# Performance work log

Hardware: AMD Instinct MI355X
Metric: run time of the kernel (lower is better)

The kernel has to match this reference:

```python
import jax, jax.numpy as jnp
import numpy as np

B, S, D = 1, 2048, 1024
F = 1408            # expert intermediate dim
E = 16              # num experts
K = 2               # top_k
CAP_FACTOR = 1.25


def _mlp(h, wg, wu, wd):
    # DeepSeek-style gated MLP (SwiGLU, no bias)
    return (jax.nn.silu(h @ wg) * (h @ wu)) @ wd


def setup_inputs() -> dict:
    key = jax.random.key(0)
    ks = jax.random.split(key, 10)
    sd = 0.02
    return {
        "x": jax.random.normal(ks[0], (B, S, D), jnp.float32),
        "router_w": jax.random.normal(ks[1], (D, E), jnp.float32) * sd,
        "router_b": jnp.zeros((E,), jnp.float32),
        "w_gate": jax.random.normal(ks[2], (E, D, F), jnp.float32) * sd,
        "w_up": jax.random.normal(ks[3], (E, D, F), jnp.float32) * sd,
        "w_down": jax.random.normal(ks[4], (E, F, D), jnp.float32) * sd,
        "sw_gate": jax.random.normal(ks[5], (D, F), jnp.float32) * sd,
        "sw_up": jax.random.normal(ks[6], (D, F), jnp.float32) * sd,
        "sw_down": jax.random.normal(ks[7], (F, D), jnp.float32) * sd,
    }


def reference(x, router_w, router_b, w_gate, w_up, w_down, sw_gate, sw_up, sw_down):
    b, s, d = x.shape
    N = b * s
    NK = N * K
    C = int(np.ceil(CAP_FACTOR * NK / E))  # per-expert capacity

    x_tokens = x.reshape(N, d)

    # Router: softmax -> top-k -> renormalize
    logits = x_tokens @ router_w + router_b           # [N, E]
    probs = jax.nn.softmax(logits, axis=-1)
    vals, idx = jax.lax.top_k(probs, K)               # [N, K]
    vals = vals / (jnp.sum(vals, axis=-1, keepdims=True) + 1e-9)
    idx_flat = idx.reshape(NK)                        # int expert ids
    vals_flat = vals.reshape(NK)

    # Position within each expert's buffer = rank in flattened (token, k) order.
    # Same math as (cumsum(one_hot)*one_hot).sum(-1)-1 in the original.
    oh_e = jax.nn.one_hot(idx_flat, E, dtype=x.dtype)             # [NK, E] (small)
    pos = (jnp.cumsum(oh_e, axis=0) * oh_e).sum(axis=1) - 1       # [NK]
    within = (pos < C).astype(x.dtype)                            # capacity mask
    pos_c = jnp.clip(pos, 0, C - 1).astype(jnp.int32)

    # Dispatch: scatter tokens into per-expert buffers. Positions are unique
    # per expert, so scatter-add equals the dense one-hot einsum exactly.
    token_ids = jnp.arange(NK) // K
    x_pair = x_tokens[token_ids] * within[:, None]                # [NK, D]
    expert_inputs = jnp.zeros((E, C, d), x.dtype).at[idx_flat, pos_c].add(x_pair)

    # Grouped expert MLPs
    expert_outputs = jax.vmap(_mlp)(expert_inputs, w_gate, w_up, w_down)  # [E, C, D]

    # Combine: gather back and weight by renormalized router probs
    gathered = expert_outputs[idx_flat, pos_c] * (vals_flat * within)[:, None]
    output_tokens = gathered.reshape(N, K, d).sum(axis=1)         # [N, D]

    return x + _mlp(x, sw_gate, sw_up, sw_down) + output_tokens.reshape(b, s, d)
```

## Files before the change

kernel.cpp:

```cpp
#include <hip/hip_runtime.h>
#include <hip/hip_bf16.h>

#define TOKENS 2048
#define DIM    1024
#define FDIM   1408
#define NEXP   16
#define NK     (TOKENS * 2)
#define CAP    320
#define RPAD   384

typedef __attribute__((ext_vector_type(4))) float f32x4;
typedef __attribute__((ext_vector_type(2))) float f32x2;
typedef __attribute__((ext_vector_type(8))) short s16x8;
typedef __attribute__((ext_vector_type(4))) short s16x4;

__device__ __forceinline__ short f2bf(float f) {
    unsigned int u = __float_as_uint(f);
    u += 0x7FFFu + ((u >> 16) & 1u);
    return (short)(u >> 16);
}
__device__ __forceinline__ float bf2f(short s) {
    return __uint_as_float(((unsigned int)(unsigned short)s) << 16);
}
__device__ __forceinline__ unsigned int f2bf_pk(float lo, float hi) {
    union { __hip_bfloat162 h; unsigned int u; } c;
    c.h = __float22bfloat162_rn(make_float2(lo, hi));
    return c.u;
}

#define GLDS16(gp, lp) __builtin_amdgcn_global_load_lds(                     \
    (const __attribute__((address_space(1))) unsigned int*)(gp),             \
    (__attribute__((address_space(3))) unsigned int*)(lp), 16, 0, 0)

struct GSegF {
    const short* A; long aStride; int aRpad;
    const float* B0; const float* B1; long bStride;
    short* Out; long oStride; int oRpad;
    const int* cnt; int Mb, Nb, N, K, nblocks;
};
struct GSegB {
    const short* A; long aStride; int aRpad;
    const short* B0; long bStride;
    short* Out; long oStride;
    const int* cnt; int Mb, Nb, N, K, nblocks;
};
struct WSeg { const float* in; short* out; int K, N, mats, nblocks; };

__device__ void wchunk_dev(const WSeg& W, int bid)
{
    const int spm = W.K >> 3;
    const int mat = bid / spm, s = bid % spm;
    const float* in  = W.in  + (size_t)mat * W.K * W.N + (size_t)s * 8 * W.N;
    short* out = W.out + (size_t)mat * W.K * W.N + (size_t)s * W.N * 8;
    const int t = threadIdx.x;
    const int iters = (W.N + 511) >> 9;
    for (int it = 0; it < iters; it++) {
        const int n = it * 512 + 2 * t;
        if (n >= W.N) break;
        const float* src = in + n;
        s16x8 o0, o1;
#pragma unroll
        for (int j = 0; j < 8; j++) {
            float2 v = *(const float2*)(src + (size_t)j * W.N);
            o0[j] = f2bf(v.x);
            o1[j] = f2bf(v.y);
        }
        *(s16x8*)(out + (size_t)n * 8)     = o0;
        *(s16x8*)(out + (size_t)n * 8 + 8) = o1;
    }
}

__device__ void router_dev(const float* __restrict__ x, const float* __restrict__ rw,
                           const float* __restrict__ rb, int* __restrict__ idx_flat,
                           float* __restrict__ vals_flat, int bid)
{
    __shared__ float lg[16][17];
    const int t  = threadIdx.x;
    const int tl = t >> 4;
    const int e  = t & 15;
    const int token = bid * 16 + tl;
    const float* xr = x + (size_t)token * DIM;

    float acc = 0.f;
    for (int d4 = 0; d4 < DIM / 4; d4++) {
        float4 xv = *(const float4*)(xr + d4 * 4);
        acc += xv.x * rw[(d4 * 4 + 0) * NEXP + e];
        acc += xv.y * rw[(d4 * 4 + 1) * NEXP + e];
        acc += xv.z * rw[(d4 * 4 + 2) * NEXP + e];
        acc += xv.w * rw[(d4 * 4 + 3) * NEXP + e];
    }
    lg[tl][e] = acc + rb[e];
    __syncthreads();

    if (t < 16) {
        float l[16];
#pragma unroll
        for (int j = 0; j < 16; j++) l[j] = lg[t][j];
        float m = l[0];
#pragma unroll
        for (int j = 1; j < 16; j++) m = fmaxf(m, l[j]);
        float p[16], den = 0.f;
#pragma unroll
        for (int j = 0; j < 16; j++) { p[j] = __expf(l[j] - m); den += p[j]; }
        int i1 = -1; float b1 = -1e30f;
#pragma unroll
        for (int j = 0; j < 16; j++) if (p[j] > b1) { b1 = p[j]; i1 = j; }
        int i2 = -1; float b2 = -1e30f;
#pragma unroll
        for (int j = 0; j < 16; j++) if (j != i1 && p[j] > b2) { b2 = p[j]; i2 = j; }
        float v1 = b1 / den, v2 = b2 / den;
        float s = v1 + v2 + 1e-9f;
        int tok = bid * 16 + t;
        idx_flat[tok * 2 + 0] = i1;
        idx_flat[tok * 2 + 1] = i2;
        vals_flat[tok * 2 + 0] = v1 / s;
        vals_flat[tok * 2 + 1] = v2 / s;
    }
}

__device__ void xconv_dev(const float* __restrict__ x, short* __restrict__ xb, int bid)
{
    const int token = bid * 2 + (threadIdx.x >> 7);
    const int c = threadIdx.x & 127;
    const float* src = x + (size_t)token * DIM + c * 8;
    float4 v0 = *(const float4*)(src);
    float4 v1 = *(const float4*)(src + 4);
    s16x8 o;
    o[0] = f2bf(v0.x); o[1] = f2bf(v0.y); o[2] = f2bf(v0.z); o[3] = f2bf(v0.w);
    o[4] = f2bf(v1.x); o[5] = f2bf(v1.y); o[6] = f2bf(v1.z); o[7] = f2bf(v1.w);
    *(s16x8*)(xb + (size_t)c * (TOKENS * 8) + (size_t)token * 8) = o;
}

__global__ __launch_bounds__(256) void rx_kernel(
    const float* __restrict__ x, const float* __restrict__ rw,
    const float* __restrict__ rb, int* __restrict__ idx_flat,
    float* __restrict__ vals, short* __restrict__ xb)
{
    int bid = blockIdx.x;
    if (bid < TOKENS / 16) { router_dev(x, rw, rb, idx_flat, vals, bid); return; }
    xconv_dev(x, xb, bid - TOKENS / 16);
}

__global__ void scan_kernel(const int* __restrict__ idx_flat,
                            const float* __restrict__ vals,
                            int* __restrict__ dst, float* __restrict__ wgt,
                            int* __restrict__ cnt)
{
    const int lane = threadIdx.x;
    int base[16];
#pragma unroll
    for (int e = 0; e < 16; e++) base[e] = 0;

    for (int c = 0; c < NK / 64; c++) {
        int i = c * 64 + lane;
        int e = idx_flat[i];
        unsigned long long m[16];
#pragma unroll
        for (int ee = 0; ee < 16; ee++) m[ee] = __ballot(e == ee);
        unsigned long long mym = 0ULL; int myb = 0;
#pragma unroll
        for (int ee = 0; ee < 16; ee++) {
            bool sel = (e == ee);
            mym = sel ? m[ee] : mym;
            myb = sel ? base[ee] : myb;
        }
        int pos = myb + (int)__popcll(mym & ((1ULL << lane) - 1ULL));
        bool within = pos < CAP;
        dst[i] = within ? (e * RPAD + pos) : -1;
        wgt[i] = within ? vals[i] : 0.f;
#pragma unroll
        for (int ee = 0; ee < 16; ee++) base[ee] += (int)__popcll(m[ee]);
    }
    if (lane < 16) cnt[lane] = base[lane] < CAP ? base[lane] : CAP;
}

__global__ __launch_bounds__(256) void scatter_kernel(
    const float* __restrict__ x, const int* __restrict__ dst,
    const int* __restrict__ idx_flat, short* __restrict__ ex)
{
    const int i = blockIdx.x * 2 + (threadIdx.x >> 7);
    const int d0 = dst[i];
    if (d0 < 0) return;
    const int e = idx_flat[i];
    const int pos = d0 - e * RPAD;
    const int token = i >> 1;
    const int c = threadIdx.x & 127;
    const float* src = x + (size_t)token * DIM + c * 8;
    float4 v0 = *(const float4*)(src);
    float4 v1 = *(const float4*)(src + 4);
    s16x8 o;
    o[0] = f2bf(v0.x); o[1] = f2bf(v0.y); o[2] = f2bf(v0.z); o[3] = f2bf(v0.w);
    o[4] = f2bf(v1.x); o[5] = f2bf(v1.y); o[6] = f2bf(v1.z); o[7] = f2bf(v1.w);
    *(s16x8*)(ex + (size_t)e * (DIM * RPAD) + (size_t)c * (RPAD * 8) +
              (size_t)pos * 8) = o;
}

template <int NMAT>
__device__ void gemm_fused_dev(const GSegF& S, int bid)
{
    constexpr int BUFS = 4096 * (1 + NMAT);
    __shared__ short lds[2 * BUFS];

    const int cpx = S.nblocks >> 3;
    const int lid = (bid & 7) * cpx + (bid >> 3);
    const int mb  = lid % S.Mb;
    const int t1  = lid / S.Mb;
    const int nb  = t1 % S.Nb;
    const int g   = t1 / S.Nb;
    const int m0 = mb * 128, n0 = nb * 128;
    if (S.cnt != nullptr && m0 >= S.cnt[g]) return;

    const int tid = threadIdx.x, lane = tid & 63, w = tid >> 6;
    const int wr = w >> 1, wc = w & 1, ln = lane & 15, kg = lane >> 4;
    const int N = S.N, K = S.K;

    const short* Ag  = S.A  + (size_t)g * S.aStride + (size_t)m0 * 8;
    const float* Bg0 = S.B0 + (size_t)g * S.bStride + n0;
    const float* Bg1 = nullptr;
    if constexpr (NMAT == 2) Bg1 = S.B1 + (size_t)g * S.bStride + n0;

    const size_t aR8 = (size_t)S.aRpad * 8;

    const int srow = tid & 127, sslab = tid >> 7;
    const short* aS0 = Ag + sslab * aR8 + srow * 8;
    const short* aS1 = Ag + (2 + sslab) * aR8 + srow * 8;
    const int dA0 = w * 512, dA1 = 2048 + w * 512;

    const float* bSrc;
    int rB, cW;
    if constexpr (NMAT == 2) {
        const int c4 = tid & 31, gq = (tid >> 5) & 3, mat = tid >> 7;
        bSrc = (mat ? Bg1 : Bg0) + (size_t)gq * 8 * N + c4 * 4;
        rB = 4096 + mat * 4096 + gq * 1024;
        cW = c4;
    } else {
        const int c2 = tid & 63, gq = tid >> 6;
        bSrc = Bg0 + (size_t)gq * 8 * N + c2 * 2;
        rB = 4096 + gq * 1024;
        cW = c2;
    }

    f32x4 bq[8];
    f32x2 bd[8];

    auto LOADB = [&](int ks) {
        const float* p = bSrc + (size_t)ks * 32 * N;
        if constexpr (NMAT == 2) {
#pragma unroll
            for (int j = 0; j < 8; j++) bq[j] = *(const f32x4*)(p + (size_t)j * N);
        } else {
#pragma unroll
            for (int j = 0; j < 8; j++) bd[j] = *(const f32x2*)(p + (size_t)j * N);
        }
    };
    auto STGA = [&](int buf, int ks) {
        const size_t ka = (size_t)ks * 4 * aR8;
        short* base = lds + buf * BUFS;
        GLDS16(aS0 + ka, base + dA0);
        GLDS16(aS1 + ka, base + dA1);
    };
    auto WRITEB = [&](int buf) {
        short* d = lds + buf * BUFS + rB;
        if constexpr (NMAT == 2) {
#pragma unroll
            for (int j = 0; j < 4; j++) {
                const int colS = (cW * 4 + j) ^ ((cW >> 1) & 7);
                uint4 o;
                o.x = f2bf_pk(bq[0][j], bq[1][j]);
                o.y = f2bf_pk(bq[2][j], bq[3][j]);
                o.z = f2bf_pk(bq[4][j], bq[5][j]);
                o.w = f2bf_pk(bq[6][j], bq[7][j]);
                *(uint4*)(d + colS * 8) = o;
            }
        } else {
#pragma unroll
            for (int j = 0; j < 2; j++) {
                const int colS = (cW * 2 + j) ^ ((cW >> 2) & 7);
                uint4 o;
                o.x = f2bf_pk(bd[0][j], bd[1][j]);
                o.y = f2bf_pk(bd[2][j], bd[3][j]);
                o.z = f2bf_pk(bd[4][j], bd[5][j]);
                o.w = f2bf_pk(bd[6][j], bd[7][j]);
                *(uint4*)(d + colS * 8) = o;
            }
        }
    };

    const int aO = kg * 1024 + (wr * 64 + ln) * 8;

    f32x4 acc[NMAT][4][4] = {};
    const int nt = K / 32;

    LOADB(0);
    __builtin_amdgcn_sched_barrier(0);
    STGA(0, 0);
    __builtin_amdgcn_sched_barrier(0);
    WRITEB(0);
    __builtin_amdgcn_sched_barrier(0);
    LOADB(1);
    __builtin_amdgcn_sched_barrier(0);
    asm volatile("s_waitcnt lgkmcnt(0)" ::: "memory");
    STGA(1, 1);
    __builtin_amdgcn_sched_barrier(0);

    int cur = 0;
    for (int ks = 0; ks < nt; ks++) {
        if (ks + 1 < nt) asm volatile("s_waitcnt vmcnt(10)" ::: "memory");
        else             asm volatile("s_waitcnt vmcnt(0)"  ::: "memory");
        __builtin_amdgcn_s_barrier();
        __builtin_amdgcn_sched_barrier(0);

        const short* base = lds + cur * BUFS;
        s16x8 af[4];
#pragma unroll
        for (int m = 0; m < 4; m++)
            af[m] = *(const s16x8*)(base + aO + m * 128);
        s16x8 bf[NMAT][4];
#pragma unroll
        for (int nf = 0; nf < 4; nf++) {
            const int col  = wc * 64 + nf * 16 + ln;
            const int colS = col ^ ((col >> 3) & 7);
#pragma unroll
            for (int mat = 0; mat < NMAT; mat++)
                bf[mat][nf] = *(const s16x8*)(base + 4096 + mat * 4096 +
                                              kg * 1024 + colS * 8);
        }

#pragma unroll
        for (int nf = 0; nf < 4; nf++)
#pragma unroll
            for (int m = 0; m < 4; m++)
#pragma unroll
                for (int mat = 0; mat < NMAT; mat++)
                    acc[mat][m][nf] = __builtin_amdgcn_mfma_f32_16x16x32_bf16(
                        af[m], bf[mat][nf], acc[mat][m][nf], 0, 0, 0);

        if (ks + 1 < nt) WRITEB(cur ^ 1);

        __builtin_amdgcn_sched_barrier(0);
        if (ks + 2 < nt) LOADB(ks + 2);
        __builtin_amdgcn_sched_barrier(0);
        asm volatile("s_waitcnt lgkmcnt(0)" ::: "memory");
        __builtin_amdgcn_s_barrier();

        if (ks + 2 < nt) {
            STGA(cur, ks + 2);
            __builtin_amdgcn_sched_barrier(0);
        }
        cur ^= 1;
    }

#pragma unroll
    for (int m = 0; m < 4; m++) {
#pragma unroll
        for (int nf = 0; nf < 4; nf++) {
            const int row = m0 + wr * 64 + m * 16 + kg * 4;
            const int col = n0 + wc * 64 + nf * 16 + ln;
#pragma unroll
            for (int j = 0; j < 4; j++) {
                if constexpr (NMAT == 2) {
                    float gv = acc[0][m][nf][j];
                    float uv = acc[1][m][nf][j];
                    float v = gv / (1.f + __expf(-gv)) * uv;
                    S.Out[(size_t)g * S.oStride + (size_t)(col >> 3) * (S.oRpad * 8) +
                          (size_t)(row + j) * 8 + (col & 7)] = f2bf(v);
                } else {
                    S.Out[(size_t)g * S.oStride + (size_t)(row + j) * N + col] =
                        f2bf(acc[0][m][nf][j]);
                }
            }
        }
    }
}

__device__ void gemm_glds64_dev(const GSegB& S, int bid)
{
    constexpr int BUFS = 6144;
    __shared__ short lds[2 * BUFS];

    const int cpx = S.nblocks >> 3;
    const int lid = (bid & 7) * cpx + (bid >> 3);
    const int mb  = lid % S.Mb;
    const int t1  = lid / S.Mb;
    const int nb  = t1 % S.Nb;
    const int g   = t1 / S.Nb;
    const int m0 = mb * 64, n0 = nb * 128;
    if (S.cnt != nullptr && m0 >= S.cnt[g]) return;

    const int tid = threadIdx.x, lane = tid & 63, w = tid >> 6;
    const int wr = w >> 1, wc = w & 1, ln = lane & 15, kg = lane >> 4;
    const int N = S.N, K = S.K;

    const short* Ag = S.A  + (size_t)g * S.aStride + (size_t)m0 * 8;
    const short* Bg = S.B0 + (size_t)g * S.bStride + (size_t)n0 * 8;

    const size_t aR8 = (size_t)S.aRpad * 8;
    const size_t n8  = (size_t)N * 8;

    const short* aS  = Ag + (size_t)(tid >> 6) * aR8 + (size_t)(tid & 63) * 8;
    const short* bS0 = Bg + (size_t)(tid >> 7) * n8 + (size_t)(tid & 127) * 8;
    const short* bS1 = Bg + (size_t)((tid >> 7) + 2) * n8 + (size_t)(tid & 127) * 8;

    const int dA  = w * 512;
    const int dB0 = 2048 + w * 512;
    const int dB1 = 4096 + w * 512;

    auto STG = [&](int buf, int ks) {
        const size_t ka = (size_t)ks * 4 * aR8;
        const size_t kb = (size_t)ks * 4 * n8;
        short* base = lds + buf * BUFS;
        GLDS16(aS + ka,  base + dA);
        GLDS16(bS0 + kb, base + dB0);
        GLDS16(bS1 + kb, base + dB1);
    };

    const int aO = kg * 512 + (wr * 32 + ln) * 8;
    const int bO = 2048 + kg * 1024 + (wc * 64 + ln) * 8;

    f32x4 acc[2][4] = {};
    const int nt = K / 32;
    STG(0, 0); STG(1, 1);
    int cur = 0;
    for (int ks = 0; ks < nt; ks++) {
        if (ks + 1 < nt) asm volatile("s_waitcnt vmcnt(3)" ::: "memory");
        else             asm volatile("s_waitcnt vmcnt(0)" ::: "memory");
        __builtin_amdgcn_s_barrier();
        __builtin_amdgcn_sched_barrier(0);

        const short* base = lds + cur * BUFS;
        s16x8 af[2];
        af[0] = *(const s16x8*)(base + aO);
        af[1] = *(const s16x8*)(base + aO + 128);
        s16x8 bf[4];
#pragma unroll
        for (int nf = 0; nf < 4; nf++)
            bf[nf] = *(const s16x8*)(base + bO + nf * 128);

#pragma unroll
        for (int nf = 0; nf < 4; nf++)
#pragma unroll
            for (int m = 0; m < 2; m++)
                acc[m][nf] = __builtin_amdgcn_mfma_f32_16x16x32_bf16(
                    af[m], bf[nf], acc[m][nf], 0, 0, 0);

        __builtin_amdgcn_sched_barrier(0);
        __builtin_amdgcn_s_barrier();
        if (ks + 2 < nt) STG(cur, ks + 2);
        cur ^= 1;
    }

#pragma unroll
    for (int m = 0; m < 2; m++) {
#pragma unroll
        for (int nf = 0; nf < 4; nf++) {
            const int row = m0 + wr * 32 + m * 16 + kg * 4;
            const int col = n0 + wc * 64 + nf * 16 + ln;
#pragma unroll
            for (int j = 0; j < 4; j++)
                S.Out[(size_t)g * S.oStride + (size_t)(row + j) * N + col] =
                    f2bf(acc[m][nf][j]);
        }
    }
}

__global__ __launch_bounds__(256, 2) void gateup_kernel(GSegF s0, GSegF s1,
                                                        WSeg w0, WSeg w1)
{
    int bid = blockIdx.x;
    if (bid < s0.nblocks) { gemm_fused_dev<2>(s0, bid); return; }
    bid -= s0.nblocks;
    if (bid < s1.nblocks) { gemm_fused_dev<2>(s1, bid); return; }
    bid -= s1.nblocks;
    if (bid < w0.nblocks) { wchunk_dev(w0, bid); return; }
    wchunk_dev(w1, bid - w0.nblocks);
}

__global__ __launch_bounds__(256, 4) void down_kernel(GSegB s0, GSegB s1)
{
    int bid = blockIdx.x;
    if (bid < s0.nblocks) { gemm_glds64_dev(s0, bid); return; }
    gemm_glds64_dev(s1, bid - s0.nblocks);
}

__global__ __launch_bounds__(256) void combine_kernel(
    const float* __restrict__ x, const short* __restrict__ shout,
    const short* __restrict__ eout, const int* __restrict__ dst,
    const float* __restrict__ wgt, float* __restrict__ out)
{
    const int t = blockIdx.x;
    const int d = threadIdx.x * 4;
    size_t o = (size_t)t * DIM + d;
    float4 xv = *(const float4*)(x + o);
    s16x4 sv = *(const s16x4*)(shout + o);
    float r0 = xv.x + bf2f(sv[0]);
    float r1 = xv.y + bf2f(sv[1]);
    float r2 = xv.z + bf2f(sv[2]);
    float r3 = xv.w + bf2f(sv[3]);
#pragma unroll
    for (int k = 0; k < 2; k++) {
        int di = dst[t * 2 + k];
        if (di >= 0) {
            float wv = wgt[t * 2 + k];
            s16x4 ev = *(const s16x4*)(eout + (size_t)di * DIM + d);
            r0 += wv * bf2f(ev[0]);
            r1 += wv * bf2f(ev[1]);
            r2 += wv * bf2f(ev[2]);
            r3 += wv * bf2f(ev[3]);
        }
    }
    float4 rv = {r0, r1, r2, r3};
    *(float4*)(out + o) = rv;
}

extern "C" void kernel_launch(void* const* d_in, const int* in_sizes, int n_in,
                              void* d_out, int out_size, void* d_ws, size_t ws_size,
                              hipStream_t stream)
{
    const float* x   = (const float*)d_in[0];
    const float* rw  = (const float*)d_in[1];
    const float* rb  = (const float*)d_in[2];
    const float* wg  = (const float*)d_in[3];
    const float* wu  = (const float*)d_in[4];
    const float* wd  = (const float*)d_in[5];
    const float* swg = (const float*)d_in[6];
    const float* swu = (const float*)d_in[7];
    const float* swd = (const float*)d_in[8];
    float* out = (float*)d_out;

    char* wp = (char*)d_ws;
    auto alloc = [&](size_t b) { char* p = wp; wp += (b + 255) & ~(size_t)255; return p; };
    int*   idx_flat = (int*)alloc((size_t)NK * 4);
    float* vals     = (float*)alloc((size_t)NK * 4);
    int*   dst      = (int*)alloc((size_t)NK * 4);
    float* wgt      = (float*)alloc((size_t)NK * 4);
    int*   cnt      = (int*)alloc(64);
    short* xb       = (short*)alloc((size_t)TOKENS * DIM * 2);
    short* ex       = (short*)alloc((size_t)NEXP * RPAD * DIM * 2);
    short* acte     = (short*)alloc((size_t)NEXP * RPAD * FDIM * 2);
    short* acts     = (short*)alloc((size_t)TOKENS * FDIM * 2);
    short* eout     = (short*)alloc((size_t)NEXP * RPAD * DIM * 2);
    short* shout    = (short*)alloc((size_t)TOKENS * DIM * 2);
    short* wdC      = (short*)alloc((size_t)NEXP * DIM * FDIM * 2);
    short* swdC     = (short*)alloc((size_t)DIM * FDIM * 2);

    rx_kernel<<<TOKENS / 16 + TOKENS / 2, 256, 0, stream>>>(x, rw, rb,
                                                            idx_flat, vals, xb);
    scan_kernel<<<1, 64, 0, stream>>>(idx_flat, vals, dst, wgt, cnt);

    scatter_kernel<<<NK / 2, 256, 0, stream>>>(x, dst, idx_flat, ex);

    GSegF segGE = {ex, (long)RPAD * DIM, RPAD, wg, wu, (long)DIM * FDIM,
                   acte, (long)RPAD * FDIM, RPAD, cnt, 3, 11, FDIM, DIM, 3 * 11 * NEXP};
    GSegF segGS = {xb, 0L, TOKENS, swg, swu, 0L,
                   acts, 0L, TOKENS, nullptr, 16, 11, FDIM, DIM, 16 * 11};
    WSeg Wd  = {wd,  wdC,  FDIM, DIM, NEXP, NEXP * (FDIM / 8)};
    WSeg Wsd = {swd, swdC, FDIM, DIM, 1,    FDIM / 8};
    gateup_kernel<<<segGE.nblocks + segGS.nblocks + Wd.nblocks + Wsd.nblocks,
                    256, 0, stream>>>(segGE, segGS, Wd, Wsd);

    GSegB segDE = {acte, (long)RPAD * FDIM, RPAD, wdC, (long)DIM * FDIM,
                   eout, (long)RPAD * DIM, cnt, 6, 8, DIM, FDIM, 6 * 8 * NEXP};
    GSegB segDS = {acts, 0L, TOKENS, swdC, 0L,
                   shout, 0L, nullptr, 32, 8, DIM, FDIM, 32 * 8};
    down_kernel<<<segDE.nblocks + segDS.nblocks, 256, 0, stream>>>(segDE, segDS);

    combine_kernel<<<TOKENS, 256, 0, stream>>>(x, shout, eout, dst, wgt, out);
}
```

Measured before the change: 230.7 us.

## Split fused gate/up GEMM into separate GEMMs plus standalone SiLU kernel

Replaces the dual-matrix fused gate/up GEMM, which computed SiLU(gate)*up in its epilogue, with single-matrix GEMMs that write gate and up results to separate bf16 buffers. A new elementwise kernel then applies SiLU and the multiply. The intent is to shrink accumulator registers and LDS per block so three blocks can fit per CU (launch bounds raised to 3). In exchange it doubles A-tile loads, adds extra global round-trips for the intermediate buffers, and adds a kernel launch.

New measurement: 259.6 us. 12.5% more time.

```diff
diff --git a/kernel.cpp b/kernel.cpp
--- a/kernel.cpp
+++ b/kernel.cpp
@@ -34,7 +34,7 @@
 
 struct GSegF {
     const short* A; long aStride; int aRpad;
-    const float* B0; const float* B1; long bStride;
+    const float* B0; long bStride;
     short* Out; long oStride; int oRpad;
     const int* cnt; int Mb, Nb, N, K, nblocks;
 };
@@ -195,10 +195,9 @@
               (size_t)pos * 8) = o;
 }
 
-template <int NMAT>
-__device__ void gemm_fused_dev(const GSegF& S, int bid)
-{
-    constexpr int BUFS = 4096 * (1 + NMAT);
+__device__ void gemm_fused1_dev(const GSegF& S, int bid)
+{
+    constexpr int BUFS = 8192;
     __shared__ short lds[2 * BUFS];
 
     const int cpx = S.nblocks >> 3;
@@ -216,8 +215,6 @@
 
     const short* Ag  = S.A  + (size_t)g * S.aStride + (size_t)m0 * 8;
     const float* Bg0 = S.B0 + (size_t)g * S.bStride + n0;
-    const float* Bg1 = nullptr;
-    if constexpr (NMAT == 2) Bg1 = S.B1 + (size_t)g * S.bStride + n0;
 
     const size_t aR8 = (size_t)S.aRpad * 8;
 
@@ -226,32 +223,16 @@
     const short* aS1 = Ag + (2 + sslab) * aR8 + srow * 8;
     const int dA0 = w * 512, dA1 = 2048 + w * 512;
 
-    const float* bSrc;
-    int rB, cW;
-    if constexpr (NMAT == 2) {
-        const int c4 = tid & 31, gq = (tid >> 5) & 3, mat = tid >> 7;
-        bSrc = (mat ? Bg1 : Bg0) + (size_t)gq * 8 * N + c4 * 4;
-        rB = 4096 + mat * 4096 + gq * 1024;
-        cW = c4;
-    } else {
-        const int c2 = tid & 63, gq = tid >> 6;
-        bSrc = Bg0 + (size_t)gq * 8 * N + c2 * 2;
-        rB = 4096 + gq * 1024;
-        cW = c2;
-    }
-
-    f32x4 bq[8];
+    const int c2 = tid & 63, gq = tid >> 6;
+    const float* bSrc = Bg0 + (size_t)gq * 8 * N + c2 * 2;
+    const int rB = 4096 + gq * 1024;
+
     f32x2 bd[8];
 
     auto LOADB = [&](int ks) {
         const float* p = bSrc + (size_t)ks * 32 * N;
-        if constexpr (NMAT == 2) {
-#pragma unroll
-            for (int j = 0; j < 8; j++) bq[j] = *(const f32x4*)(p + (size_t)j * N);
-        } else {
-#pragma unroll
-            for (int j = 0; j < 8; j++) bd[j] = *(const f32x2*)(p + (size_t)j * N);
-        }
+#pragma unroll
+        for (int j = 0; j < 8; j++) bd[j] = *(const f32x2*)(p + (size_t)j * N);
     };
     auto STGA = [&](int buf, int ks) {
         const size_t ka = (size_t)ks * 4 * aR8;
@@ -261,34 +242,21 @@
     };
     auto WRITEB = [&](int buf) {
         short* d = lds + buf * BUFS + rB;
-        if constexpr (NMAT == 2) {
-#pragma unroll
-            for (int j = 0; j < 4; j++) {
-                const int colS = (cW * 4 + j) ^ ((cW >> 1) & 7);
-                uint4 o;
-                o.x = f2bf_pk(bq[0][j], bq[1][j]);
-                o.y = f2bf_pk(bq[2][j], bq[3][j]);
-                o.z = f2bf_pk(bq[4][j], bq[5][j]);
-                o.w = f2bf_pk(bq[6][j], bq[7][j]);
-                *(uint4*)(d + colS * 8) = o;
-            }
-        } else {
-#pragma unroll
-            for (int j = 0; j < 2; j++) {
-                const int colS = (cW * 2 + j) ^ ((cW >> 2) & 7);
-                uint4 o;
-                o.x = f2bf_pk(bd[0][j], bd[1][j]);
-                o.y = f2bf_pk(bd[2][j], bd[3][j]);
-                o.z = f2bf_pk(bd[4][j], bd[5][j]);
-                o.w = f2bf_pk(bd[6][j], bd[7][j]);
-                *(uint4*)(d + colS * 8) = o;
-            }
+#pragma unroll
+        for (int j = 0; j < 2; j++) {
+            const int colS = (c2 * 2 + j) ^ ((c2 >> 2) & 7);
+            uint4 o;
+            o.x = f2bf_pk(bd[0][j], bd[1][j]);
+            o.y = f2bf_pk(bd[2][j], bd[3][j]);
+            o.z = f2bf_pk(bd[4][j], bd[5][j]);
+            o.w = f2bf_pk(bd[6][j], bd[7][j]);
+            *(uint4*)(d + colS * 8) = o;
         }
     };
 
     const int aO = kg * 1024 + (wr * 64 + ln) * 8;
 
-    f32x4 acc[NMAT][4][4] = {};
+    f32x4 acc[4][4] = {};
     const int nt = K / 32;
 
     LOADB(0);
@@ -315,25 +283,20 @@
 #pragma unroll
         for (int m = 0; m < 4; m++)
             af[m] = *(const s16x8*)(base + aO + m * 128);
-        s16x8 bf[NMAT][4];
+        s16x8 bf[4];
 #pragma unroll
         for (int nf = 0; nf < 4; nf++) {
             const int col  = wc * 64 + nf * 16 + ln;
             const int colS = col ^ ((col >> 3) & 7);
-#pragma unroll
-            for (int mat = 0; mat < NMAT; mat++)
-                bf[mat][nf] = *(const s16x8*)(base + 4096 + mat * 4096 +
-                                              kg * 1024 + colS * 8);
+            bf[nf] = *(const s16x8*)(base + 4096 + kg * 1024 + colS * 8);
         }
 
 #pragma unroll
         for (int nf = 0; nf < 4; nf++)
 #pragma unroll
             for (int m = 0; m < 4; m++)
-#pragma unroll
-                for (int mat = 0; mat < NMAT; mat++)
-                    acc[mat][m][nf] = __builtin_amdgcn_mfma_f32_16x16x32_bf16(
-                        af[m], bf[mat][nf], acc[mat][m][nf], 0, 0, 0);
+                acc[m][nf] = __builtin_amdgcn_mfma_f32_16x16x32_bf16(
+                    af[m], bf[nf], acc[m][nf], 0, 0, 0);
 
         if (ks + 1 < nt) WRITEB(cur ^ 1);
 
@@ -357,20 +320,33 @@
             const int row = m0 + wr * 64 + m * 16 + kg * 4;
             const int col = n0 + wc * 64 + nf * 16 + ln;
 #pragma unroll
-            for (int j = 0; j < 4; j++) {
-                if constexpr (NMAT == 2) {
-                    float gv = acc[0][m][nf][j];
-                    float uv = acc[1][m][nf][j];
-                    float v = gv / (1.f + __expf(-gv)) * uv;
-                    S.Out[(size_t)g * S.oStride + (size_t)(col >> 3) * (S.oRpad * 8) +
-                          (size_t)(row + j) * 8 + (col & 7)] = f2bf(v);
-                } else {
-                    S.Out[(size_t)g * S.oStride + (size_t)(row + j) * N + col] =
-                        f2bf(acc[0][m][nf][j]);
-                }
-            }
-        }
-    }
+            for (int j = 0; j < 4; j++)
+                S.Out[(size_t)g * S.oStride + (size_t)(col >> 3) * (S.oRpad * 8) +
+                      (size_t)(row + j) * 8 + (col & 7)] = f2bf(acc[m][nf][j]);
+        }
+    }
+}
+
+__global__ __launch_bounds__(256) void silu_kernel(
+    const short* __restrict__ g0, const short* __restrict__ u0,
+    short* __restrict__ o0, long n0,
+    const short* __restrict__ g1, const short* __restrict__ u1,
+    short* __restrict__ o1)
+{
+    size_t i = ((size_t)blockIdx.x * 256 + threadIdx.x) * 8;
+    const short *gp, *up; short* op;
+    if (i < (size_t)n0) { gp = g0 + i; up = u0 + i; op = o0 + i; }
+    else { i -= n0; gp = g1 + i; up = u1 + i; op = o1 + i; }
+    s16x8 gv = *(const s16x8*)gp;
+    s16x8 uv = *(const s16x8*)up;
+    s16x8 o;
+#pragma unroll
+    for (int j = 0; j < 8; j++) {
+        float gf = bf2f(gv[j]);
+        float uf = bf2f(uv[j]);
+        o[j] = f2bf(gf / (1.f + __expf(-gf)) * uf);
+    }
+    *(s16x8*)op = o;
 }
 
 __device__ void gemm_glds64_dev(const GSegB& S, int bid)
@@ -463,14 +439,18 @@
     }
 }
 
-__global__ __launch_bounds__(256, 2) void gateup_kernel(GSegF s0, GSegF s1,
-                                                        WSeg w0, WSeg w1)
+__global__ __launch_bounds__(256, 3) void gateup_kernel(
+    GSegF s0, GSegF s1, GSegF s2, GSegF s3, WSeg w0, WSeg w1)
 {
     int bid = blockIdx.x;
-    if (bid < s0.nblocks) { gemm_fused_dev<2>(s0, bid); return; }
+    if (bid < s0.nblocks) { gemm_fused1_dev(s0, bid); return; }
     bid -= s0.nblocks;
-    if (bid < s1.nblocks) { gemm_fused_dev<2>(s1, bid); return; }
+    if (bid < s1.nblocks) { gemm_fused1_dev(s1, bid); return; }
     bid -= s1.nblocks;
+    if (bid < s2.nblocks) { gemm_fused1_dev(s2, bid); return; }
+    bid -= s2.nblocks;
+    if (bid < s3.nblocks) { gemm_fused1_dev(s3, bid); return; }
+    bid -= s3.nblocks;
     if (bid < w0.nblocks) { wchunk_dev(w0, bid); return; }
     wchunk_dev(w1, bid - w0.nblocks);
 }
@@ -536,6 +516,10 @@
     int*   cnt      = (int*)alloc(64);
     short* xb       = (short*)alloc((size_t)TOKENS * DIM * 2);
     short* ex       = (short*)alloc((size_t)NEXP * RPAD * DIM * 2);
+    short* gE       = (short*)alloc((size_t)NEXP * RPAD * FDIM * 2);
+    short* uE       = (short*)alloc((size_t)NEXP * RPAD * FDIM * 2);
+    short* gS       = (short*)alloc((size_t)TOKENS * FDIM * 2);
+    short* uS       = (short*)alloc((size_t)TOKENS * FDIM * 2);
     short* acte     = (short*)alloc((size_t)NEXP * RPAD * FDIM * 2);
     short* acts     = (short*)alloc((size_t)TOKENS * FDIM * 2);
     short* eout     = (short*)alloc((size_t)NEXP * RPAD * DIM * 2);
@@ -549,14 +533,24 @@
 
     scatter_kernel<<<NK / 2, 256, 0, stream>>>(x, dst, idx_flat, ex);
 
-    GSegF segGE = {ex, (long)RPAD * DIM, RPAD, wg, wu, (long)DIM * FDIM,
-                   acte, (long)RPAD * FDIM, RPAD, cnt, 3, 11, FDIM, DIM, 3 * 11 * NEXP};
-    GSegF segGS = {xb, 0L, TOKENS, swg, swu, 0L,
-                   acts, 0L, TOKENS, nullptr, 16, 11, FDIM, DIM, 16 * 11};
+    GSegF segGe = {ex, (long)RPAD * DIM, RPAD, wg, (long)DIM * FDIM,
+                   gE, (long)RPAD * FDIM, RPAD, cnt, 3, 11, FDIM, DIM, 3 * 11 * NEXP};
+    GSegF segUe = {ex, (long)RPAD * DIM, RPAD, wu, (long)DIM * FDIM,
+                   uE, (long)RPAD * FDIM, RPAD, cnt, 3, 11, FDIM, DIM, 3 * 11 * NEXP};
+    GSegF segGs = {xb, 0L, TOKENS, swg, 0L,
+                   gS, 0L, TOKENS, nullptr, 16, 11, FDIM, DIM, 16 * 11};
+    GSegF segUs = {xb, 0L, TOKENS, swu, 0L,
+                   uS, 0L, TOKENS, nullptr, 16, 11, FDIM, DIM, 16 * 11};
     WSeg Wd  = {wd,  wdC,  FDIM, DIM, NEXP, NEXP * (FDIM / 8)};
     WSeg Wsd = {swd, swdC, FDIM, DIM, 1,    FDIM / 8};
-    gateup_kernel<<<segGE.nblocks + segGS.nblocks + Wd.nblocks + Wsd.nblocks,
-                    256, 0, stream>>>(segGE, segGS, Wd, Wsd);
+    gateup_kernel<<<segGe.nblocks + segUe.nblocks + segGs.nblocks +
+                    segUs.nblocks + Wd.nblocks + Wsd.nblocks,
+                    256, 0, stream>>>(segGe, segUe, segGs, segUs, Wd, Wsd);
+
+    const long nE = (long)NEXP * RPAD * FDIM;
+    const long nS = (long)TOKENS * FDIM;
+    silu_kernel<<<(int)((nE + nS) / 8 / 256), 256, 0, stream>>>(
+        gE, uE, acte, nE, gS, uS, acts);
 
     GSegB segDE = {acte, (long)RPAD * FDIM, RPAD, wdC, (long)DIM * FDIM,
                    eout, (long)RPAD * DIM, cnt, 6, 8, DIM, FDIM, 6 * 8 * NEXP};
```
